# Kernel tuning notes

Hardware: AMD Instinct MI355X
Metric: run time of the kernel (lower is better)

## Reference

```python
import jax, jax.numpy as jnp
import numpy as np

EPS = 1e-8

def _dwconv1d(x, w, b):
    # x: [B, C, T], w: [C, 1, K] depthwise, b: [C]; 'same' padding
    y = jax.lax.conv_general_dilated(
        x, w, window_strides=(1,), padding='SAME',
        dimension_numbers=('NCH', 'OIH', 'NCH'),
        feature_group_count=x.shape[1])
    return y + b[None, :, None]

def _conv1d(x, w, b):
    # x: [B, 1, T], w: [1, 1, K], b: [1]
    y = jax.lax.conv_general_dilated(
        x, w, window_strides=(1,), padding='SAME',
        dimension_numbers=('NCH', 'OIH', 'NCH'))
    return y + b[None, :, None]

def setup_inputs() -> dict:
    key = jax.random.key(0)
    ks = jax.random.split(key, 8)
    B, F, T = 4, 256, 60000
    N_bands, N_diff, N_la, N_g, sigma_g = 8, 5, 11, 15, 3.0
    x = jax.random.uniform(ks[0], (B, F, T), dtype=jnp.float32)
    log_gamma = jnp.full((N_bands,), jnp.log(10.0), dtype=jnp.float32)
    # diff kernel: [-1, +1] centered, depthwise conv2d weight [8,1,1,5]
    dk = np.zeros((N_bands, 1, 1, N_diff), dtype=np.float32)
    dk[..., N_diff // 2] = -1.0
    dk[..., N_diff // 2 + 1] = 1.0
    diff_w = jnp.asarray(dk)
    diff_b = 0.01 * jax.random.normal(ks[1], (N_bands,), dtype=jnp.float32)
    la_w = jnp.ones((N_bands, 1, N_la), dtype=jnp.float32) / N_la
    la_b = 0.01 * jax.random.normal(ks[2], (N_bands,), dtype=jnp.float32)
    mix_w = jnp.ones((1, N_bands), dtype=jnp.float32) / N_bands
    gwin = jnp.exp(-(jnp.arange(N_g, dtype=jnp.float32) - N_g // 2) ** 2 / (2.0 * sigma_g))
    g_w = gwin.reshape(1, 1, -1)
    g_b = 0.01 * jax.random.normal(ks[3], (1,), dtype=jnp.float32)
    fc_w = jnp.ones((1, 4), dtype=jnp.float32) / 4.0
    fc_b = 0.01 * jax.random.normal(ks[4], (1,), dtype=jnp.float32)
    fg_w = gwin.reshape(1, 1, -1)
    fg_b = 0.01 * jax.random.normal(ks[5], (1,), dtype=jnp.float32)
    return dict(x=x, log_gamma=log_gamma, diff_w=diff_w, diff_b=diff_b,
                la_w=la_w, la_b=la_b, mix_w=mix_w, g_w=g_w, g_b=g_b,
                fc_w=fc_w, fc_b=fc_b, fg_w=fg_w, fg_b=fg_b)

def reference(x, log_gamma, diff_w, diff_b, la_w, la_b, mix_w, g_w, g_b,
              fc_w, fc_b, fg_w, fg_b):
    B, F, T = x.shape
    NB = log_gamma.shape[0]  # 8 bands
    Fb = F // NB
    # chunk(dim=1)+stack(dim=3)+permute(0,3,1,2) == reshape to [B, NB, Fb, T]
    xr = x.reshape(B, NB, Fb, T)
    # logarithmic compression, gamma per band
    xl = jnp.log1p(jnp.exp(log_gamma)[None, :, None, None] * xr)
    # depthwise temporal differentiation, kernel (1, N_diff), 'same'
    xd = jax.lax.conv_general_dilated(
        xl, diff_w, window_strides=(1, 1), padding='SAME',
        dimension_numbers=('NCHW', 'OIHW', 'NCHW'),
        feature_group_count=NB) + diff_b[None, :, None, None]
    # half-wave rectification (LeakyReLU, slope 0.0)
    xh = jax.nn.leaky_relu(xd, negative_slope=0.0)
    # pool over frequency -> [B, NB, T]
    xp = xh.sum(axis=2)
    # subtract local average (depthwise conv1d, ones/11)
    xs = xp - _dwconv1d(xp, la_w, la_b)
    # weighted sum over bands (Linear, no bias) -> [B, 1, T]
    xm = jnp.einsum('bct,oc->bot', xs, mix_w)
    # gaussian smoothing -> [B, T]
    xg = _conv1d(xm, g_w, g_b)[:, 0, :]
    xg = jax.nn.leaky_relu(xg, negative_slope=0.0)
    spectral_flux = xg / (xg.max(axis=1, keepdims=True) + EPS)
    # Fuser: concat 4 copies of spectral_flux along last axis -> [B, T, 4]
    conc = jnp.stack([spectral_flux] * 4, axis=-1)
    fm = jnp.einsum('btc,oc->bto', conc, fc_w) + fc_b  # [B, T, 1]
    fs = _conv1d(fm.transpose(0, 2, 1), fg_w, fg_b)    # [B, 1, T]
    fa = jax.nn.sigmoid(fs[:, 0, :])
    fused_nov = fa / (fa.max(axis=1, keepdims=True) + EPS)
    return spectral_flux, fused_nov
```

## Files before the change

kernel.cpp:

```cpp
#include <hip/hip_runtime.h>
#include <cmath>

#define T_LEN 60000
#define BATCH 4
#define NBANDS 8
#define FB 32
#define EPS 1e-8f

#define K1_TILE 496
#define K1_ROWLEN 512
#define K1_NBX ((T_LEN + K1_TILE - 1) / K1_TILE)

__global__ __launch_bounds__(256) void k1_xp(
        const float* __restrict__ x, const float* __restrict__ log_gamma,
        const float* __restrict__ diff_w, const float* __restrict__ diff_b,
        float* __restrict__ xp, int* __restrict__ mslots) {
    extern __shared__ float sh[];
    const int tid = threadIdx.x;
    const int bx = blockIdx.x, band = blockIdx.y, b = blockIdx.z;
    if (bx == 0 && band == 0 && b == 0 && tid < 8)
        mslots[tid] = 0;
    const int tile0 = bx * K1_TILE;
    const int w0 = tile0 - 8;
    const float* base = x + ((size_t)((b * NBANDS + band) * FB)) * T_LEN;
    const bool interior = (w0 >= 0) && (w0 + K1_ROWLEN <= T_LEN);
    if (interior) {
#pragma unroll
        for (int c = 0; c < 16; ++c) {
            const int idx = c * 1024 + tid * 4;
            const int r = idx >> 9;
            const int i = idx & 511;
            float4 v = *(const float4*)(base + (size_t)r * T_LEN + w0 + i);
            *(float4*)&sh[idx] = v;
        }
    } else {
        for (int c = 0; c < 16; ++c) {
            const int idx = c * 1024 + tid * 4;
            const int r = idx >> 9;
            const int i = idx & 511;
            const float* rowp = base + (size_t)r * T_LEN;
#pragma unroll
            for (int j = 0; j < 4; ++j) {
                const int t = w0 + i + j;
                sh[idx + j] = (t >= 0 && t < T_LEN) ? rowp[t] : 0.f;
            }
        }
    }
    __syncthreads();
    const float gamma = __expf(log_gamma[band]);
    float dw[5];
#pragma unroll
    for (int k = 0; k < 5; ++k) dw[k] = diff_w[band * 5 + k];
    const float db = diff_b[band];
    const int t0 = tile0 + 2 * tid;
    if (tid < 248 && t0 < T_LEN) {
        float acc0 = 0.f, acc1 = 0.f;
        const int i0 = 2 * tid + 6;
#pragma unroll 4
        for (int r = 0; r < FB; ++r) {
            const float* rp = &sh[r * K1_ROWLEN];
            float2 pa = *(const float2*)(rp + i0);
            float2 pb = *(const float2*)(rp + i0 + 2);
            float2 pc = *(const float2*)(rp + i0 + 4);
            float e0 = __logf(fmaf(gamma, pa.x, 1.f));
            float e1 = __logf(fmaf(gamma, pa.y, 1.f));
            float e2 = __logf(fmaf(gamma, pb.x, 1.f));
            float e3 = __logf(fmaf(gamma, pb.y, 1.f));
            float e4 = __logf(fmaf(gamma, pc.x, 1.f));
            float e5 = __logf(fmaf(gamma, pc.y, 1.f));
            float xd0 = db, xd1 = db;
            xd0 = fmaf(dw[0], e0, xd0); xd1 = fmaf(dw[0], e1, xd1);
            xd0 = fmaf(dw[1], e1, xd0); xd1 = fmaf(dw[1], e2, xd1);
            xd0 = fmaf(dw[2], e2, xd0); xd1 = fmaf(dw[2], e3, xd1);
            xd0 = fmaf(dw[3], e3, xd0); xd1 = fmaf(dw[3], e4, xd1);
            xd0 = fmaf(dw[4], e4, xd0); xd1 = fmaf(dw[4], e5, xd1);
            acc0 += fmaxf(xd0, 0.f);
            acc1 += fmaxf(xd1, 0.f);
        }
        float* op = xp + ((size_t)(b * NBANDS + band)) * T_LEN + t0;
        op[0] = acc0;
        if (t0 + 1 < T_LEN) op[1] = acc1;
    }
}

#define K2_STAGE 288
__global__ __launch_bounds__(256) void k2_xg(
        const float* __restrict__ xp,
        const float* __restrict__ la_w, const float* __restrict__ la_b,
        const float* __restrict__ mix_w, const float* __restrict__ g_w,
        const float* __restrict__ g_b,
        float* __restrict__ xg, int* __restrict__ m1_bits) {
    __shared__ float sh[NBANDS][K2_STAGE];
    __shared__ float H[NBANDS][25];
    __shared__ float red[4];
    const int tid = threadIdx.x;
    const int T0 = blockIdx.x * 256;
    const int b = blockIdx.y;
    const float* xpb = xp + (size_t)b * NBANDS * T_LEN;
    for (int idx = tid; idx < NBANDS * (K2_STAGE / 4); idx += 256) {
        int c = idx / (K2_STAGE / 4);
        int i4 = idx % (K2_STAGE / 4);
        int g = T0 - 16 + 4 * i4;
        const float* rowp = xpb + (size_t)c * T_LEN;
        float4 v;
        if (g >= 0 && g + 3 < T_LEN) {
            v = *(const float4*)(rowp + g);
        } else {
            v.x = (g + 0 >= 0 && g + 0 < T_LEN) ? rowp[g + 0] : 0.f;
            v.y = (g + 1 >= 0 && g + 1 < T_LEN) ? rowp[g + 1] : 0.f;
            v.z = (g + 2 >= 0 && g + 2 < T_LEN) ? rowp[g + 2] : 0.f;
            v.w = (g + 3 >= 0 && g + 3 < T_LEN) ? rowp[g + 3] : 0.f;
        }
        *(float4*)&sh[c][4 * i4] = v;
    }
    if (tid < 200) {
        int c = tid / 25, m = tid % 25;
        int klo = m - 14 > 0 ? m - 14 : 0;
        int khi = m < 10 ? m : 10;
        float mw = mix_w[c], s = 0.f;
        for (int k = klo; k <= khi; ++k)
            s += g_w[m - k] * (mw * ((k == 5 ? 1.f : 0.f) - la_w[c * 11 + k]));
        H[c][m] = s;
    }
    float Sg = 0.f;
#pragma unroll
    for (int j = 0; j < 15; ++j) Sg += g_w[j];
    float C0 = 0.f;
#pragma unroll
    for (int c = 0; c < NBANDS; ++c) C0 -= mix_w[c] * la_b[c];
    const float cst = g_b[0] + Sg * C0;
    __syncthreads();
    const int t = T0 + tid;
    float v = cst;
#pragma unroll 1
    for (int c = 0; c < NBANDS; ++c) {
        float a = 0.f;
#pragma unroll
        for (int m = 0; m < 25; ++m) a = fmaf(H[c][m], sh[c][tid + 4 + m], a);
        v += a;
    }
    if (t < 7 || (t >= T_LEN - 7 && t < T_LEN)) {
        v = g_b[0];
        for (int jj = 0; jj < 15; ++jj) {
            int tp = t + jj - 7;
            if (tp < 0 || tp >= T_LEN) continue;
            float xm = C0;
            for (int c = 0; c < NBANDS; ++c) {
                float mw = mix_w[c];
                for (int k = 0; k < 11; ++k) {
                    int i = tp + k + 11 - T0;
                    xm = fmaf(mw * ((k == 5 ? 1.f : 0.f) - la_w[c * 11 + k]),
                              sh[c][i], xm);
                }
            }
            v = fmaf(g_w[jj], xm, v);
        }
    }
    float vmax = 0.f;
    if (t < T_LEN) {
        v = fmaxf(v, 0.f);
        xg[(size_t)b * T_LEN + t] = v;
        vmax = v;
    }
#pragma unroll
    for (int off = 32; off > 0; off >>= 1) vmax = fmaxf(vmax, __shfl_down(vmax, off));
    if ((tid & 63) == 0) red[tid >> 6] = vmax;
    __syncthreads();
    if (tid == 0) {
        float m = fmaxf(fmaxf(red[0], red[1]), fmaxf(red[2], red[3]));
        atomicMax(&m1_bits[b], __float_as_int(m));
    }
}

__global__ __launch_bounds__(256) void k3a(
        const float* __restrict__ xg, const int* __restrict__ m1_bits,
        const float* __restrict__ fc_w, const float* __restrict__ fc_b,
        const float* __restrict__ fg_w, const float* __restrict__ fg_b,
        float* __restrict__ sf_out, float* __restrict__ fa_out,
        int* __restrict__ m2_bits) {
    __shared__ float shfm[272];
    __shared__ float red[4];
    const int tid = threadIdx.x;
    const int t0 = blockIdx.x * 256;
    const int b = blockIdx.y;
    const float inv = 1.f / (__int_as_float(m1_bits[b]) + EPS);
    const float sfc = fc_w[0] + fc_w[1] + fc_w[2] + fc_w[3];
    const float fcb = fc_b[0];
    for (int i = tid; i < 270; i += 256) {
        int tt = t0 + i - 7;
        float v = 0.f;
        if (tt >= 0 && tt < T_LEN)
            v = fmaf(sfc, xg[(size_t)b * T_LEN + tt] * inv, fcb);
        shfm[i] = v;
    }
    __syncthreads();
    const int t = t0 + tid;
    float fs = fg_b[0];
#pragma unroll
    for (int k = 0; k < 15; ++k) fs = fmaf(fg_w[k], shfm[tid + k], fs);
    float sig = 1.f / (1.f + __expf(-fs));
    float v;
    if (t < T_LEN) {
        sf_out[(size_t)b * T_LEN + t] = xg[(size_t)b * T_LEN + t] * inv;
        fa_out[(size_t)b * T_LEN + t] = sig;
        v = sig;
    } else {
        v = 0.f;
    }
#pragma unroll
    for (int off = 32; off > 0; off >>= 1) v = fmaxf(v, __shfl_down(v, off));
    if ((tid & 63) == 0) red[tid >> 6] = v;
    __syncthreads();
    if (tid == 0) {
        float m = fmaxf(fmaxf(red[0], red[1]), fmaxf(red[2], red[3]));
        atomicMax(&m2_bits[b], __float_as_int(m));
    }
}

__global__ void k3b(float* __restrict__ fa, const int* __restrict__ m2_bits) {
    int idx = blockIdx.x * 256 + threadIdx.x;
    if (idx >= BATCH * T_LEN) return;
    int b = idx / T_LEN;
    float inv = 1.f / (__int_as_float(m2_bits[b]) + EPS);
    fa[idx] = fa[idx] * inv;
}

extern "C" void kernel_launch(void* const* d_in, const int* in_sizes, int n_in,
                              void* d_out, int out_size, void* d_ws, size_t ws_size,
                              hipStream_t stream) {
    const float* x    = (const float*)d_in[0];
    const float* lg   = (const float*)d_in[1];
    const float* dw   = (const float*)d_in[2];
    const float* db   = (const float*)d_in[3];
    const float* law  = (const float*)d_in[4];
    const float* lab  = (const float*)d_in[5];
    const float* mixw = (const float*)d_in[6];
    const float* gw   = (const float*)d_in[7];
    const float* gb   = (const float*)d_in[8];
    const float* fcw  = (const float*)d_in[9];
    const float* fcb  = (const float*)d_in[10];
    const float* fgw  = (const float*)d_in[11];
    const float* fgb  = (const float*)d_in[12];

    float* ws = (float*)d_ws;
    float* xp = ws;
    float* xg = ws + (size_t)BATCH * NBANDS * T_LEN;
    int*   m1 = (int*)(xg + (size_t)BATCH * T_LEN);

    float* sf_out = (float*)d_out;
    float* fn_out = sf_out + (size_t)BATCH * T_LEN;

    const int tb256 = (T_LEN + 255) / 256;

    k1_xp<<<dim3(K1_NBX, NBANDS, BATCH), dim3(256),
            FB * K1_ROWLEN * sizeof(float), stream>>>(
        x, lg, dw, db, xp, m1);
    k2_xg<<<dim3(tb256, BATCH), dim3(256), 0, stream>>>(
        xp, law, lab, mixw, gw, gb, xg, m1);
    k3a<<<dim3(tb256, BATCH), dim3(256), 0, stream>>>(
        xg, m1, fcw, fcb, fgw, fgb, sf_out, fn_out, m1 + 4);
    k3b<<<dim3((BATCH * T_LEN + 255) / 256), dim3(256), 0, stream>>>(fn_out, m1 + 4);
}
```

Before: 414.7 us.

## Fuse post-processing kernels into one cooperative kernel with grid syncs

Merges the smoothing, normalisation, fuser conv and final max-normalisation kernels into one cooperative launch. Grid-wide syncs stand in for the kernel boundaries around the two per-batch max reductions. The block's xg values stay in shared memory, so only halo values are read back from global, and the sigmoid output is held in a register instead of being written and then rescaled in place. This removes two launches and some global traffic. The cost is that every block (235x4) must be resident at once for the cooperative launch, plus two grid barriers.

New measurement: 558.6 us. 1.35x slower.

```diff
diff --git a/kernel.cpp b/kernel.cpp
--- a/kernel.cpp
+++ b/kernel.cpp
@@ -1,5 +1,8 @@
 #include <hip/hip_runtime.h>
+#include <hip/hip_cooperative_groups.h>
 #include <cmath>
+
+namespace cg = cooperative_groups;
 
 #define T_LEN 60000
 #define BATCH 4
@@ -84,19 +87,26 @@
 }
 
 #define K2_STAGE 288
-__global__ __launch_bounds__(256) void k2_xg(
+__global__ __launch_bounds__(256) void k23_fused(
         const float* __restrict__ xp,
         const float* __restrict__ la_w, const float* __restrict__ la_b,
         const float* __restrict__ mix_w, const float* __restrict__ g_w,
         const float* __restrict__ g_b,
-        float* __restrict__ xg, int* __restrict__ m1_bits) {
+        float* __restrict__ xg, int* __restrict__ m1_bits,
+        const float* __restrict__ fc_w, const float* __restrict__ fc_b,
+        const float* __restrict__ fg_w, const float* __restrict__ fg_b,
+        float* __restrict__ sf_out, float* __restrict__ fn_out,
+        int* __restrict__ m2_bits) {
     __shared__ float sh[NBANDS][K2_STAGE];
     __shared__ float H[NBANDS][25];
     __shared__ float red[4];
+    __shared__ float xgs[256];
+    __shared__ float shfm[272];
     const int tid = threadIdx.x;
     const int T0 = blockIdx.x * 256;
     const int b = blockIdx.y;
     const float* xpb = xp + (size_t)b * NBANDS * T_LEN;
+
     for (int idx = tid; idx < NBANDS * (K2_STAGE / 4); idx += 256) {
         int c = idx / (K2_STAGE / 4);
         int i4 = idx % (K2_STAGE / 4);
@@ -161,6 +171,9 @@
         v = fmaxf(v, 0.f);
         xg[(size_t)b * T_LEN + t] = v;
         vmax = v;
+        xgs[tid] = v;
+    } else {
+        xgs[tid] = 0.f;
     }
 #pragma unroll
     for (int off = 32; off > 0; off >>= 1) vmax = fmaxf(vmax, __shfl_down(vmax, off));
@@ -170,59 +183,50 @@
         float m = fmaxf(fmaxf(red[0], red[1]), fmaxf(red[2], red[3]));
         atomicMax(&m1_bits[b], __float_as_int(m));
     }
-}
-
-__global__ __launch_bounds__(256) void k3a(
-        const float* __restrict__ xg, const int* __restrict__ m1_bits,
-        const float* __restrict__ fc_w, const float* __restrict__ fc_b,
-        const float* __restrict__ fg_w, const float* __restrict__ fg_b,
-        float* __restrict__ sf_out, float* __restrict__ fa_out,
-        int* __restrict__ m2_bits) {
-    __shared__ float shfm[272];
-    __shared__ float red[4];
-    const int tid = threadIdx.x;
-    const int t0 = blockIdx.x * 256;
-    const int b = blockIdx.y;
+
+    cg::this_grid().sync();
+
     const float inv = 1.f / (__int_as_float(m1_bits[b]) + EPS);
     const float sfc = fc_w[0] + fc_w[1] + fc_w[2] + fc_w[3];
     const float fcb = fc_b[0];
     for (int i = tid; i < 270; i += 256) {
-        int tt = t0 + i - 7;
-        float v = 0.f;
-        if (tt >= 0 && tt < T_LEN)
-            v = fmaf(sfc, xg[(size_t)b * T_LEN + tt] * inv, fcb);
-        shfm[i] = v;
-    }
-    __syncthreads();
-    const int t = t0 + tid;
+        int tt = T0 + i - 7;
+        float fmv = 0.f;
+        if (tt >= 0 && tt < T_LEN) {
+            float xv = (tt >= T0 && tt < T0 + 256)
+                           ? xgs[tt - T0]
+                           : xg[(size_t)b * T_LEN + tt];
+            fmv = fmaf(sfc, xv * inv, fcb);
+        }
+        shfm[i] = fmv;
+    }
+    __syncthreads();
     float fs = fg_b[0];
 #pragma unroll
     for (int k = 0; k < 15; ++k) fs = fmaf(fg_w[k], shfm[tid + k], fs);
     float sig = 1.f / (1.f + __expf(-fs));
-    float v;
+    float v2;
     if (t < T_LEN) {
-        sf_out[(size_t)b * T_LEN + t] = xg[(size_t)b * T_LEN + t] * inv;
-        fa_out[(size_t)b * T_LEN + t] = sig;
-        v = sig;
+        sf_out[(size_t)b * T_LEN + t] = xgs[tid] * inv;
+        v2 = sig;
     } else {
-        v = 0.f;
-    }
-#pragma unroll
-    for (int off = 32; off > 0; off >>= 1) v = fmaxf(v, __shfl_down(v, off));
-    if ((tid & 63) == 0) red[tid >> 6] = v;
+        v2 = 0.f;
+    }
+#pragma unroll
+    for (int off = 32; off > 0; off >>= 1) v2 = fmaxf(v2, __shfl_down(v2, off));
+    if ((tid & 63) == 0) red[tid >> 6] = v2;
     __syncthreads();
     if (tid == 0) {
         float m = fmaxf(fmaxf(red[0], red[1]), fmaxf(red[2], red[3]));
         atomicMax(&m2_bits[b], __float_as_int(m));
     }
-}
-
-__global__ void k3b(float* __restrict__ fa, const int* __restrict__ m2_bits) {
-    int idx = blockIdx.x * 256 + threadIdx.x;
-    if (idx >= BATCH * T_LEN) return;
-    int b = idx / T_LEN;
-    float inv = 1.f / (__int_as_float(m2_bits[b]) + EPS);
-    fa[idx] = fa[idx] * inv;
+
+    cg::this_grid().sync();
+
+    if (t < T_LEN) {
+        const float inv2 = 1.f / (__int_as_float(m2_bits[b]) + EPS);
+        fn_out[(size_t)b * T_LEN + t] = sig * inv2;
+    }
 }
 
 extern "C" void kernel_launch(void* const* d_in, const int* in_sizes, int n_in,
@@ -246,6 +250,7 @@
     float* xp = ws;
     float* xg = ws + (size_t)BATCH * NBANDS * T_LEN;
     int*   m1 = (int*)(xg + (size_t)BATCH * T_LEN);
+    int*   m2 = m1 + 4;
 
     float* sf_out = (float*)d_out;
     float* fn_out = sf_out + (size_t)BATCH * T_LEN;
@@ -255,9 +260,12 @@
     k1_xp<<<dim3(K1_NBX, NBANDS, BATCH), dim3(256),
             FB * K1_ROWLEN * sizeof(float), stream>>>(
         x, lg, dw, db, xp, m1);
-    k2_xg<<<dim3(tb256, BATCH), dim3(256), 0, stream>>>(
-        xp, law, lab, mixw, gw, gb, xg, m1);
-    k3a<<<dim3(tb256, BATCH), dim3(256), 0, stream>>>(
-        xg, m1, fcw, fcb, fgw, fgb, sf_out, fn_out, m1 + 4);
-    k3b<<<dim3((BATCH * T_LEN + 255) / 256), dim3(256), 0, stream>>>(fn_out, m1 + 4);
+
+    void* args[] = {
+        (void*)&xp, (void*)&law, (void*)&lab, (void*)&mixw, (void*)&gw,
+        (void*)&gb, (void*)&xg, (void*)&m1, (void*)&fcw, (void*)&fcb,
+        (void*)&fgw, (void*)&fgb, (void*)&sf_out, (void*)&fn_out, (void*)&m2
+    };
+    hipLaunchCooperativeKernel((void*)k23_fused, dim3(tb256, BATCH), dim3(256),
+                               args, 0, stream);
 }
```

## Drop LDS staging in k1 and compute four outputs per thread from global

Applied to the files above, without the earlier changes.

The first kernel no longer stages a 32x512 tile in shared memory. Each thread now loads overlapping float2 windows straight from global memory and computes four diff/rectify outputs per row, then writes them with one float4 store. This removes the 64KB LDS allocation that limited occupancy, and it cuts the redundant halo logarithms from three per output to two. In exchange the overlapping loads depend on the cache, and there is a separate scalar path for edge threads.

New measurement: 423.7 us. +2.2%, slower.

```diff
diff --git a/kernel.cpp b/kernel.cpp
--- a/kernel.cpp
+++ b/kernel.cpp
@@ -7,80 +7,86 @@
 #define FB 32
 #define EPS 1e-8f
 
-#define K1_TILE 496
-#define K1_ROWLEN 512
-#define K1_NBX ((T_LEN + K1_TILE - 1) / K1_TILE)
+#define K1_TPB 256
+#define K1_SPAN (K1_TPB * 4)
+#define K1_NBX ((T_LEN + K1_SPAN - 1) / K1_SPAN)
 
 __global__ __launch_bounds__(256) void k1_xp(
         const float* __restrict__ x, const float* __restrict__ log_gamma,
         const float* __restrict__ diff_w, const float* __restrict__ diff_b,
         float* __restrict__ xp, int* __restrict__ mslots) {
-    extern __shared__ float sh[];
     const int tid = threadIdx.x;
     const int bx = blockIdx.x, band = blockIdx.y, b = blockIdx.z;
     if (bx == 0 && band == 0 && b == 0 && tid < 8)
         mslots[tid] = 0;
-    const int tile0 = bx * K1_TILE;
-    const int w0 = tile0 - 8;
-    const float* base = x + ((size_t)((b * NBANDS + band) * FB)) * T_LEN;
-    const bool interior = (w0 >= 0) && (w0 + K1_ROWLEN <= T_LEN);
-    if (interior) {
-#pragma unroll
-        for (int c = 0; c < 16; ++c) {
-            const int idx = c * 1024 + tid * 4;
-            const int r = idx >> 9;
-            const int i = idx & 511;
-            float4 v = *(const float4*)(base + (size_t)r * T_LEN + w0 + i);
-            *(float4*)&sh[idx] = v;
-        }
-    } else {
-        for (int c = 0; c < 16; ++c) {
-            const int idx = c * 1024 + tid * 4;
-            const int r = idx >> 9;
-            const int i = idx & 511;
-            const float* rowp = base + (size_t)r * T_LEN;
-#pragma unroll
-            for (int j = 0; j < 4; ++j) {
-                const int t = w0 + i + j;
-                sh[idx + j] = (t >= 0 && t < T_LEN) ? rowp[t] : 0.f;
-            }
-        }
-    }
-    __syncthreads();
+    const int t0 = bx * K1_SPAN + tid * 4;
+    if (t0 >= T_LEN) return;
     const float gamma = __expf(log_gamma[band]);
     float dw[5];
 #pragma unroll
     for (int k = 0; k < 5; ++k) dw[k] = diff_w[band * 5 + k];
     const float db = diff_b[band];
-    const int t0 = tile0 + 2 * tid;
-    if (tid < 248 && t0 < T_LEN) {
-        float acc0 = 0.f, acc1 = 0.f;
-        const int i0 = 2 * tid + 6;
+    const float* base = x + ((size_t)((b * NBANDS + band) * FB)) * T_LEN;
+    float acc0 = 0.f, acc1 = 0.f, acc2 = 0.f, acc3 = 0.f;
+    const bool interior = (t0 >= 2) && (t0 + 6 <= T_LEN);
+    if (interior) {
+        const float* rp = base + t0;
 #pragma unroll 4
+        for (int r = 0; r < FB; ++r, rp += T_LEN) {
+            float2 va = *(const float2*)(rp - 2);
+            float2 vb = *(const float2*)(rp);
+            float2 vc = *(const float2*)(rp + 2);
+            float2 vd = *(const float2*)(rp + 4);
+            float e0 = __logf(fmaf(gamma, va.x, 1.f));
+            float e1 = __logf(fmaf(gamma, va.y, 1.f));
+            float e2 = __logf(fmaf(gamma, vb.x, 1.f));
+            float e3 = __logf(fmaf(gamma, vb.y, 1.f));
+            float e4 = __logf(fmaf(gamma, vc.x, 1.f));
+            float e5 = __logf(fmaf(gamma, vc.y, 1.f));
+            float e6 = __logf(fmaf(gamma, vd.x, 1.f));
+            float e7 = __logf(fmaf(gamma, vd.y, 1.f));
+            float x0 = db, x1 = db, x2 = db, x3 = db;
+            x0 = fmaf(dw[0], e0, x0); x1 = fmaf(dw[0], e1, x1);
+            x2 = fmaf(dw[0], e2, x2); x3 = fmaf(dw[0], e3, x3);
+            x0 = fmaf(dw[1], e1, x0); x1 = fmaf(dw[1], e2, x1);
+            x2 = fmaf(dw[1], e3, x2); x3 = fmaf(dw[1], e4, x3);
+            x0 = fmaf(dw[2], e2, x0); x1 = fmaf(dw[2], e3, x1);
+            x2 = fmaf(dw[2], e4, x2); x3 = fmaf(dw[2], e5, x3);
+            x0 = fmaf(dw[3], e3, x0); x1 = fmaf(dw[3], e4, x1);
+            x2 = fmaf(dw[3], e5, x2); x3 = fmaf(dw[3], e6, x3);
+            x0 = fmaf(dw[4], e4, x0); x1 = fmaf(dw[4], e5, x1);
+            x2 = fmaf(dw[4], e6, x2); x3 = fmaf(dw[4], e7, x3);
+            acc0 += fmaxf(x0, 0.f);
+            acc1 += fmaxf(x1, 0.f);
+            acc2 += fmaxf(x2, 0.f);
+            acc3 += fmaxf(x3, 0.f);
+        }
+    } else {
+        float acc[4] = {0.f, 0.f, 0.f, 0.f};
         for (int r = 0; r < FB; ++r) {
-            const float* rp = &sh[r * K1_ROWLEN];
-            float2 pa = *(const float2*)(rp + i0);
-            float2 pb = *(const float2*)(rp + i0 + 2);
-            float2 pc = *(const float2*)(rp + i0 + 4);
-            float e0 = __logf(fmaf(gamma, pa.x, 1.f));
-            float e1 = __logf(fmaf(gamma, pa.y, 1.f));
-            float e2 = __logf(fmaf(gamma, pb.x, 1.f));
-            float e3 = __logf(fmaf(gamma, pb.y, 1.f));
-            float e4 = __logf(fmaf(gamma, pc.x, 1.f));
-            float e5 = __logf(fmaf(gamma, pc.y, 1.f));
-            float xd0 = db, xd1 = db;
-            xd0 = fmaf(dw[0], e0, xd0); xd1 = fmaf(dw[0], e1, xd1);
-            xd0 = fmaf(dw[1], e1, xd0); xd1 = fmaf(dw[1], e2, xd1);
-            xd0 = fmaf(dw[2], e2, xd0); xd1 = fmaf(dw[2], e3, xd1);
-            xd0 = fmaf(dw[3], e3, xd0); xd1 = fmaf(dw[3], e4, xd1);
-            xd0 = fmaf(dw[4], e4, xd0); xd1 = fmaf(dw[4], e5, xd1);
-            acc0 += fmaxf(xd0, 0.f);
-            acc1 += fmaxf(xd1, 0.f);
-        }
-        float* op = xp + ((size_t)(b * NBANDS + band)) * T_LEN + t0;
-        op[0] = acc0;
-        if (t0 + 1 < T_LEN) op[1] = acc1;
-    }
+            const float* rowp = base + (size_t)r * T_LEN;
+            float e[8];
+#pragma unroll
+            for (int j = 0; j < 8; ++j) {
+                int t = t0 + j - 2;
+                float xv = (t >= 0 && t < T_LEN) ? rowp[t] : 0.f;
+                e[j] = __logf(fmaf(gamma, xv, 1.f));
+            }
+#pragma unroll
+            for (int j = 0; j < 4; ++j) {
+                float xd = db;
+                xd = fmaf(dw[0], e[j + 0], xd);
+                xd = fmaf(dw[1], e[j + 1], xd);
+                xd = fmaf(dw[2], e[j + 2], xd);
+                xd = fmaf(dw[3], e[j + 3], xd);
+                xd = fmaf(dw[4], e[j + 4], xd);
+                acc[j] += fmaxf(xd, 0.f);
+            }
+        }
+        acc0 = acc[0]; acc1 = acc[1]; acc2 = acc[2]; acc3 = acc[3];
+    }
+    float4 o; o.x = acc0; o.y = acc1; o.z = acc2; o.w = acc3;
+    *(float4*)(xp + ((size_t)(b * NBANDS + band)) * T_LEN + t0) = o;
 }
 
 #define K2_STAGE 288
@@ -252,8 +258,7 @@
 
     const int tb256 = (T_LEN + 255) / 256;
 
-    k1_xp<<<dim3(K1_NBX, NBANDS, BATCH), dim3(256),
-            FB * K1_ROWLEN * sizeof(float), stream>>>(
+    k1_xp<<<dim3(K1_NBX, NBANDS, BATCH), dim3(256), 0, stream>>>(
         x, lg, dw, db, xp, m1);
     k2_xg<<<dim3(tb256, BATCH), dim3(256), 0, stream>>>(
         xp, law, lab, mixw, gw, gb, xg, m1);
```

## Fold fuser smoothing into xg kernel and derive sigmoid max analytically

Applied to the files above, without the earlier changes.

The xg kernel now computes xg over a haloed tile. It also computes the unnormalised Gaussian-smoothed signal G and reduces its per-batch max, storing the boundary values separately. Because the fuser is affine in xg and sigmoid is monotone, the final kernel can get the fused-novelty max in closed form from max(G) and the edge values. That removes the separate normalisation pass over fa and one kernel launch. In exchange it adds extra halo work and an extra workspace write/read of G, and correctness depends on the scale factor being positive.

After: 408.4 us. About the same (-1.5%).

```diff
diff --git a/kernel.cpp b/kernel.cpp
--- a/kernel.cpp
+++ b/kernel.cpp
@@ -83,16 +83,20 @@
     }
 }
 
-#define K2_STAGE 288
+#define K2_STAGE 296
+#define XGE_N 270
 __global__ __launch_bounds__(256) void k2_xg(
         const float* __restrict__ xp,
         const float* __restrict__ la_w, const float* __restrict__ la_b,
         const float* __restrict__ mix_w, const float* __restrict__ g_w,
-        const float* __restrict__ g_b,
-        float* __restrict__ xg, int* __restrict__ m1_bits) {
+        const float* __restrict__ g_b, const float* __restrict__ fg_w,
+        float* __restrict__ xg, float* __restrict__ Gws,
+        int* __restrict__ m1_bits, int* __restrict__ mG_bits,
+        float* __restrict__ Gb) {
     __shared__ float sh[NBANDS][K2_STAGE];
     __shared__ float H[NBANDS][25];
-    __shared__ float red[4];
+    __shared__ float xge[XGE_N];
+    __shared__ float redV[4], redG[4];
     const int tid = threadIdx.x;
     const int T0 = blockIdx.x * 256;
     const int b = blockIdx.y;
@@ -100,7 +104,7 @@
     for (int idx = tid; idx < NBANDS * (K2_STAGE / 4); idx += 256) {
         int c = idx / (K2_STAGE / 4);
         int i4 = idx % (K2_STAGE / 4);
-        int g = T0 - 16 + 4 * i4;
+        int g = T0 - 20 + 4 * i4;
         const float* rowp = xpb + (size_t)c * T_LEN;
         float4 v;
         if (g >= 0 && g + 3 < T_LEN) {
@@ -128,101 +132,128 @@
     float C0 = 0.f;
 #pragma unroll
     for (int c = 0; c < NBANDS; ++c) C0 -= mix_w[c] * la_b[c];
-    const float cst = g_b[0] + Sg * C0;
-    __syncthreads();
+    const float g_b0 = g_b[0];
+    const float cst = g_b0 + Sg * C0;
+    __syncthreads();
+
+    auto compute_xg = [&](int p) -> float {
+        const int t = T0 - 7 + p;
+        if (t < 0 || t >= T_LEN) return 0.f;
+        float v = cst;
+#pragma unroll 1
+        for (int c = 0; c < NBANDS; ++c) {
+            float a = 0.f;
+#pragma unroll
+            for (int m = 0; m < 25; ++m) a = fmaf(H[c][m], sh[c][p + 1 + m], a);
+            v += a;
+        }
+        if (t < 7 || t >= T_LEN - 7) {
+            v = g_b0;
+            for (int jj = 0; jj < 15; ++jj) {
+                int tp = t + jj - 7;
+                if (tp < 0 || tp >= T_LEN) continue;
+                float xm = C0;
+                for (int c = 0; c < NBANDS; ++c) {
+                    float mw = mix_w[c];
+                    for (int k = 0; k < 11; ++k) {
+                        int i = tp + k + 15 - T0;
+                        xm = fmaf(mw * ((k == 5 ? 1.f : 0.f) - la_w[c * 11 + k]),
+                                  sh[c][i], xm);
+                    }
+                }
+                v = fmaf(g_w[jj], xm, v);
+            }
+        }
+        return fmaxf(v, 0.f);
+    };
+    xge[tid] = compute_xg(tid);
+    if (tid < XGE_N - 256) xge[256 + tid] = compute_xg(256 + tid);
+    __syncthreads();
+
     const int t = T0 + tid;
-    float v = cst;
-#pragma unroll 1
-    for (int c = 0; c < NBANDS; ++c) {
-        float a = 0.f;
-#pragma unroll
-        for (int m = 0; m < 25; ++m) a = fmaf(H[c][m], sh[c][tid + 4 + m], a);
-        v += a;
-    }
-    if (t < 7 || (t >= T_LEN - 7 && t < T_LEN)) {
-        v = g_b[0];
-        for (int jj = 0; jj < 15; ++jj) {
-            int tp = t + jj - 7;
-            if (tp < 0 || tp >= T_LEN) continue;
-            float xm = C0;
-            for (int c = 0; c < NBANDS; ++c) {
-                float mw = mix_w[c];
-                for (int k = 0; k < 11; ++k) {
-                    int i = tp + k + 11 - T0;
-                    xm = fmaf(mw * ((k == 5 ? 1.f : 0.f) - la_w[c * 11 + k]),
-                              sh[c][i], xm);
-                }
-            }
-            v = fmaf(g_w[jj], xm, v);
-        }
-    }
-    float vmax = 0.f;
+    const float xv = xge[tid + 7];
+    float G = 0.f;
+#pragma unroll
+    for (int k = 0; k < 15; ++k) G = fmaf(fg_w[k], xge[tid + k], G);
+    float vmax = 0.f, gmax = 0.f;
     if (t < T_LEN) {
-        v = fmaxf(v, 0.f);
-        xg[(size_t)b * T_LEN + t] = v;
-        vmax = v;
-    }
-#pragma unroll
-    for (int off = 32; off > 0; off >>= 1) vmax = fmaxf(vmax, __shfl_down(vmax, off));
-    if ((tid & 63) == 0) red[tid >> 6] = vmax;
+        xg[(size_t)b * T_LEN + t] = xv;
+        Gws[(size_t)b * T_LEN + t] = G;
+        vmax = xv;
+        if (t >= 7 && t < T_LEN - 7) gmax = G;
+        else {
+            int j = (t < 7) ? t : (t - (T_LEN - 7) + 7);
+            Gb[b * 14 + j] = G;
+        }
+    }
+#pragma unroll
+    for (int off = 32; off > 0; off >>= 1) {
+        vmax = fmaxf(vmax, __shfl_down(vmax, off));
+        gmax = fmaxf(gmax, __shfl_down(gmax, off));
+    }
+    if ((tid & 63) == 0) { redV[tid >> 6] = vmax; redG[tid >> 6] = gmax; }
     __syncthreads();
     if (tid == 0) {
-        float m = fmaxf(fmaxf(red[0], red[1]), fmaxf(red[2], red[3]));
-        atomicMax(&m1_bits[b], __float_as_int(m));
-    }
-}
-
-__global__ __launch_bounds__(256) void k3a(
-        const float* __restrict__ xg, const int* __restrict__ m1_bits,
+        float mv = fmaxf(fmaxf(redV[0], redV[1]), fmaxf(redV[2], redV[3]));
+        float mg = fmaxf(fmaxf(redG[0], redG[1]), fmaxf(redG[2], redG[3]));
+        atomicMax(&m1_bits[b], __float_as_int(mv));
+        atomicMax(&mG_bits[b], __float_as_int(mg));
+    }
+}
+
+__global__ __launch_bounds__(256) void k3(
+        const float* __restrict__ xg, const float* __restrict__ Gws,
+        const int* __restrict__ m1_bits, const int* __restrict__ mG_bits,
+        const float* __restrict__ Gb,
         const float* __restrict__ fc_w, const float* __restrict__ fc_b,
         const float* __restrict__ fg_w, const float* __restrict__ fg_b,
-        float* __restrict__ sf_out, float* __restrict__ fa_out,
-        int* __restrict__ m2_bits) {
-    __shared__ float shfm[272];
-    __shared__ float red[4];
+        float* __restrict__ sf_out, float* __restrict__ fn_out) {
     const int tid = threadIdx.x;
-    const int t0 = blockIdx.x * 256;
+    const int t = blockIdx.x * 256 + tid;
     const int b = blockIdx.y;
+    if (t >= T_LEN) return;
     const float inv = 1.f / (__int_as_float(m1_bits[b]) + EPS);
     const float sfc = fc_w[0] + fc_w[1] + fc_w[2] + fc_w[3];
     const float fcb = fc_b[0];
-    for (int i = tid; i < 270; i += 256) {
-        int tt = t0 + i - 7;
-        float v = 0.f;
-        if (tt >= 0 && tt < T_LEN)
-            v = fmaf(sfc, xg[(size_t)b * T_LEN + tt] * inv, fcb);
-        shfm[i] = v;
-    }
-    __syncthreads();
-    const int t = t0 + tid;
-    float fs = fg_b[0];
-#pragma unroll
-    for (int k = 0; k < 15; ++k) fs = fmaf(fg_w[k], shfm[tid + k], fs);
-    float sig = 1.f / (1.f + __expf(-fs));
-    float v;
-    if (t < T_LEN) {
-        sf_out[(size_t)b * T_LEN + t] = xg[(size_t)b * T_LEN + t] * inv;
-        fa_out[(size_t)b * T_LEN + t] = sig;
-        v = sig;
+    const float fgb = fg_b[0];
+    const float s = sfc * inv;
+    float ps[15];
+    {
+        float a = 0.f;
+#pragma unroll
+        for (int k = 0; k < 15; ++k) { a += fg_w[k]; ps[k] = a; }
+    }
+    const float Sfg = ps[14];
+    const float C1i = fmaf(fcb, Sfg, fgb);
+    float fsmax = fmaf(s, __int_as_float(mG_bits[b]), C1i);
+#pragma unroll
+    for (int j = 0; j < 7; ++j) {
+        float W = Sfg - ps[6 - j];
+        fsmax = fmaxf(fsmax, fmaf(s, Gb[b * 14 + j], fmaf(fcb, W, fgb)));
+    }
+#pragma unroll
+    for (int j = 0; j < 7; ++j) {
+        float W = ps[13 - j];
+        fsmax = fmaxf(fsmax, fmaf(s, Gb[b * 14 + 7 + j], fmaf(fcb, W, fgb)));
+    }
+    const float m2 = 1.f / (1.f + __expf(-fsmax));
+    const float inv2 = 1.f / (m2 + EPS);
+    float W_own;
+    if (t >= 7 && t < T_LEN - 7) {
+        W_own = Sfg;
     } else {
-        v = 0.f;
-    }
-#pragma unroll
-    for (int off = 32; off > 0; off >>= 1) v = fmaxf(v, __shfl_down(v, off));
-    if ((tid & 63) == 0) red[tid >> 6] = v;
-    __syncthreads();
-    if (tid == 0) {
-        float m = fmaxf(fmaxf(red[0], red[1]), fmaxf(red[2], red[3]));
-        atomicMax(&m2_bits[b], __float_as_int(m));
-    }
-}
-
-__global__ void k3b(float* __restrict__ fa, const int* __restrict__ m2_bits) {
-    int idx = blockIdx.x * 256 + threadIdx.x;
-    if (idx >= BATCH * T_LEN) return;
-    int b = idx / T_LEN;
-    float inv = 1.f / (__int_as_float(m2_bits[b]) + EPS);
-    fa[idx] = fa[idx] * inv;
+        W_own = 0.f;
+        for (int k = 0; k < 15; ++k) {
+            int tp = t - 7 + k;
+            if (tp >= 0 && tp < T_LEN) W_own += fg_w[k];
+        }
+    }
+    const float G = Gws[(size_t)b * T_LEN + t];
+    const float fs = fmaf(s, G, fmaf(fcb, W_own, fgb));
+    const float sig = 1.f / (1.f + __expf(-fs));
+    const float xv = xg[(size_t)b * T_LEN + t];
+    sf_out[(size_t)b * T_LEN + t] = xv * inv;
+    fn_out[(size_t)b * T_LEN + t] = sig * inv2;
 }
 
 extern "C" void kernel_launch(void* const* d_in, const int* in_sizes, int n_in,
@@ -244,8 +275,11 @@
 
     float* ws = (float*)d_ws;
     float* xp = ws;
-    float* xg = ws + (size_t)BATCH * NBANDS * T_LEN;
-    int*   m1 = (int*)(xg + (size_t)BATCH * T_LEN);
+    float* xg = xp + (size_t)BATCH * NBANDS * T_LEN;
+    float* Gw = xg + (size_t)BATCH * T_LEN;
+    int*   m1 = (int*)(Gw + (size_t)BATCH * T_LEN);
+    int*   mG = m1 + 4;
+    float* Gb = (float*)(mG + 4);
 
     float* sf_out = (float*)d_out;
     float* fn_out = sf_out + (size_t)BATCH * T_LEN;
@@ -256,8 +290,7 @@
             FB * K1_ROWLEN * sizeof(float), stream>>>(
         x, lg, dw, db, xp, m1);
     k2_xg<<<dim3(tb256, BATCH), dim3(256), 0, stream>>>(
-        xp, law, lab, mixw, gw, gb, xg, m1);
-    k3a<<<dim3(tb256, BATCH), dim3(256), 0, stream>>>(
-        xg, m1, fcw, fcb, fgw, fgb, sf_out, fn_out, m1 + 4);
-    k3b<<<dim3((BATCH * T_LEN + 255) / 256), dim3(256), 0, stream>>>(fn_out, m1 + 4);
-}
+        xp, law, lab, mixw, gw, gb, fgw, xg, Gw, m1, mG, Gb);
+    k3<<<dim3(tb256, BATCH), dim3(256), 0, stream>>>(
+        xg, Gw, m1, mG, Gb, fcw, fcb, fgw, fgb, sf_out, fn_out);
+}
```
